# Optimization experiments

Measured on AMD Instinct MI355X. Metric: run time of the kernel, lower is better.

Reference implementation:

```python
import jax, jax.numpy as jnp
import numpy as np

# dims: T tokens, HID hidden, H heads, D head_dim, K conv kernel size
T, HID, H, D, K = 4096, 2048, 16, 128, 4
HD = H * D
EPS = 1e-6


def causal_conv(x, w):
    # depthwise causal conv: x [T, C], w [C, K]; y_t = sum_i w[:, i] * x_{t-K+1+i}
    xp = jnp.pad(x, ((K - 1, 0), (0, 0)))
    y = jnp.zeros_like(x)
    for i in range(K):  # small fixed kernel loop
        y = y + w[:, i] * xp[i:i + x.shape[0]]
    return y


def l2norm(x):
    return x * jax.lax.rsqrt(jnp.sum(x * x, -1, keepdims=True) + EPS)


def setup_inputs() -> dict:
    key = jax.random.key(0)
    ks = jax.random.split(key, 16)
    s = lambda n: 1.0 / np.sqrt(n)
    return {
        "hidden_states": jax.random.normal(ks[0], (T, HID), jnp.float32),
        "Wq": jax.random.normal(ks[1], (HID, HD), jnp.float32) * s(HID),
        "Wk": jax.random.normal(ks[2], (HID, HD), jnp.float32) * s(HID),
        "Wv": jax.random.normal(ks[3], (HID, HD), jnp.float32) * s(HID),
        "wq_conv": jax.random.normal(ks[4], (HD, K), jnp.float32) * s(K),
        "wk_conv": jax.random.normal(ks[5], (HD, K), jnp.float32) * s(K),
        "wv_conv": jax.random.normal(ks[6], (HD, K), jnp.float32) * s(K),
        "A_log": jax.random.uniform(ks[7], (H,), jnp.float32, 0.0, 0.5),
        "dt_bias": jax.random.normal(ks[8], (HD,), jnp.float32) * 0.1,
        "Wfa": jax.random.normal(ks[9], (HID, D), jnp.float32) * s(HID),
        "Wfb": jax.random.normal(ks[10], (D, HD), jnp.float32) * s(D),
        "Wb": jax.random.normal(ks[11], (HID, H), jnp.float32) * s(HID),
        "Wga": jax.random.normal(ks[12], (HID, D), jnp.float32) * s(HID),
        "Wgb": jax.random.normal(ks[13], (D, HD), jnp.float32) * s(D),
        "norm_w": jnp.ones((D,), jnp.float32),
        "Wo": jax.random.normal(ks[14], (HD, HID), jnp.float32) * s(HD),
    }


def reference(hidden_states, Wq, Wk, Wv, wq_conv, wk_conv, wv_conv, A_log,
              dt_bias, Wfa, Wfb, Wb, Wga, Wgb, norm_w, Wo):
    x = hidden_states
    # projections + short causal conv + SiLU
    q = jax.nn.silu(causal_conv(x @ Wq, wq_conv)).reshape(T, H, D)
    k = jax.nn.silu(causal_conv(x @ Wk, wk_conv)).reshape(T, H, D)
    v = jax.nn.silu(causal_conv(x @ Wv, wv_conv)).reshape(T, H, D)
    # fine-grained per-channel log-decay: g = -exp(A_log) * softplus(f + dt_bias), [T,H,D]
    f = (x @ Wfa) @ Wfb + dt_bias
    g = -(jnp.exp(A_log)[None, :, None]) * jax.nn.softplus(f.reshape(T, H, D))
    beta = jax.nn.sigmoid(x @ Wb)  # [T, H]
    q = l2norm(q)
    k = l2norm(k)
    scale = D ** -0.5

    def step(S, inp):  # S: [H, Dk, Dv]
        q_t, k_t, v_t, g_t, b_t = inp
        S = S * jnp.exp(g_t)[..., None]  # diagonal per-key-channel decay
        err = v_t - jnp.einsum('hkv,hk->hv', S, k_t)  # delta-rule error
        dv = b_t[:, None] * err  # beta gate
        S = S + k_t[:, :, None] * dv[:, None, :]
        o_t = jnp.einsum('hkv,hk->hv', S, q_t) * scale
        return S, o_t

    S0 = jnp.zeros((H, D, D), jnp.float32)
    _, o = jax.lax.scan(step, S0, (q, k, v, g, beta))  # o: [T, H, D]

    # gated RMSNorm then output projection
    gate = ((x @ Wga) @ Wgb).reshape(T, H, D)
    o = o * jax.lax.rsqrt(jnp.mean(o * o, -1, keepdims=True) + EPS)
    o = o * norm_w * jax.nn.silu(gate)
    return o.reshape(T, HD) @ Wo
```

## Files before the change

kernel.cpp:

```cpp
#include <hip/hip_runtime.h>
#include <hip/hip_bf16.h>
#include <math.h>

typedef __bf16 bf16_t;
typedef __bf16 bf16x8 __attribute__((ext_vector_type(8)));
typedef float  floatx4 __attribute__((ext_vector_type(4)));
typedef float  floatx2 __attribute__((ext_vector_type(2)));
typedef unsigned uintx4 __attribute__((ext_vector_type(4)));

constexpr int T_TOK = 4096;
constexpr int HID   = 2048;
constexpr int NH    = 16;
constexpr int DH    = 128;
constexpr int CH    = 2048;
constexpr int CHUNK = 16;
constexpr int NCH   = T_TOK / CHUNK;

__global__ __launch_bounds__(256) void cast_to_bf16(const float* __restrict__ in,
                                                    bf16_t* __restrict__ out, int n) {
  int i = (blockIdx.x * 256 + threadIdx.x) * 8;
  if (i >= n) return;
  float4 a = *(const float4*)(in + i);
  float4 b = *(const float4*)(in + i + 4);
  bf16x8 o;
  o[0]=(bf16_t)a.x; o[1]=(bf16_t)a.y; o[2]=(bf16_t)a.z; o[3]=(bf16_t)a.w;
  o[4]=(bf16_t)b.x; o[5]=(bf16_t)b.y; o[6]=(bf16_t)b.z; o[7]=(bf16_t)b.w;
  *(bf16x8*)(out + i) = o;
}

__global__ __launch_bounds__(256) void transpose_cast(const float* __restrict__ in,
                                                      bf16_t* __restrict__ out, int R, int C) {
  __shared__ float tile[32][33];
  int tx = threadIdx.x & 31;
  int ty = threadIdx.x >> 5;
  int r0 = blockIdx.x * 32;
  int c0 = blockIdx.y * 32;
#pragma unroll
  for (int i = 0; i < 4; i++) {
    int r = ty + i * 8;
    float v = 0.f;
    if (r0 + r < R && c0 + tx < C) v = in[(size_t)(r0 + r) * C + (c0 + tx)];
    tile[r][tx] = v;
  }
  __syncthreads();
#pragma unroll
  for (int i = 0; i < 4; i++) {
    int cr = ty + i * 8;
    if (c0 + cr < C && r0 + tx < R)
      out[(size_t)(c0 + cr) * R + (r0 + tx)] = (bf16_t)tile[tx][cr];
  }
}

template<bool OUT_BF16>
__global__ __launch_bounds__(256) void gemm_bf16(
    const bf16_t* __restrict__ A, int lda,
    const bf16_t* __restrict__ Bt, int ldb,
    void* __restrict__ Cv, int ldc, int M, int N, int K) {
  __shared__ bf16_t sA[128][40];
  __shared__ bf16_t sB[128][40];
  const int tid  = threadIdx.x;
  const int bm0  = blockIdx.x * 128;
  const int bn0  = blockIdx.y * 128;
  const int wave = tid >> 6;
  const int lane = tid & 63;
  const int wm   = (wave & 1) * 64;
  const int wn   = (wave >> 1) * 64;
  const int fm   = lane & 15;
  const int kq   = lane >> 4;

  floatx4 acc[4][4];
#pragma unroll
  for (int mi = 0; mi < 4; mi++)
#pragma unroll
    for (int ni = 0; ni < 4; ni++)
      acc[mi][ni] = (floatx4){0.f, 0.f, 0.f, 0.f};

  const int sr = tid >> 2;
  const int sk = (tid & 3) * 8;
  const bool bval0 = (bn0 + sr) < N;
  const bool bval1 = (bn0 + sr + 64) < N;
  const bf16_t* Ag0 = A + (size_t)(bm0 + sr) * lda + sk;
  const bf16_t* Ag1 = Ag0 + (size_t)64 * lda;
  const bf16_t* Bg0 = Bt + (size_t)(bn0 + sr) * ldb + sk;
  const bf16_t* Bg1 = Bg0 + (size_t)64 * ldb;

  for (int k0 = 0; k0 < K; k0 += 32) {
    float4 a0 = *(const float4*)(Ag0 + k0);
    float4 a1 = *(const float4*)(Ag1 + k0);
    float4 b0 = bval0 ? *(const float4*)(Bg0 + k0) : make_float4(0.f, 0.f, 0.f, 0.f);
    float4 b1 = bval1 ? *(const float4*)(Bg1 + k0) : make_float4(0.f, 0.f, 0.f, 0.f);
    __syncthreads();
    *(float4*)(&sA[sr][sk])      = a0;
    *(float4*)(&sA[sr + 64][sk]) = a1;
    *(float4*)(&sB[sr][sk])      = b0;
    *(float4*)(&sB[sr + 64][sk]) = b1;
    __syncthreads();
    bf16x8 afr[4], bfr[4];
#pragma unroll
    for (int i = 0; i < 4; i++) {
      afr[i] = *(const bf16x8*)(&sA[wm + i * 16 + fm][kq * 8]);
      bfr[i] = *(const bf16x8*)(&sB[wn + i * 16 + fm][kq * 8]);
    }
#pragma unroll
    for (int mi = 0; mi < 4; mi++)
#pragma unroll
      for (int ni = 0; ni < 4; ni++)
        acc[mi][ni] = __builtin_amdgcn_mfma_f32_16x16x32_bf16(afr[mi], bfr[ni], acc[mi][ni], 0, 0, 0);
  }

  const int rr = (lane >> 4) * 4;
#pragma unroll
  for (int mi = 0; mi < 4; mi++) {
#pragma unroll
    for (int r = 0; r < 4; r++) {
      const int row = bm0 + wm + mi * 16 + rr + r;
#pragma unroll
      for (int ni = 0; ni < 4; ni++) {
        const int col = bn0 + wn + ni * 16 + fm;
        if (col < N) {
          if constexpr (OUT_BF16)
            ((bf16_t*)Cv)[(size_t)row * ldc + col] = (bf16_t)acc[mi][ni][r];
          else
            ((float*)Cv)[(size_t)row * ldc + col] = acc[mi][ni][r];
        }
      }
    }
  }
}

template<bool L2NORM>
__global__ __launch_bounds__(256) void conv_silu(
    const bf16_t* __restrict__ raw, const float* __restrict__ wconv,
    bf16_t* __restrict__ out) {
  const int t   = blockIdx.x;
  const int tid = threadIdx.x;
  const int c0  = tid * 8;

  float w[8][4];
#pragma unroll
  for (int j = 0; j < 8; j++) {
    float4 t0 = *(const float4*)(wconv + (size_t)(c0 + j) * 4);
    w[j][0] = t0.x; w[j][1] = t0.y; w[j][2] = t0.z; w[j][3] = t0.w;
  }
  float a[8] = {};
#pragma unroll
  for (int i = 0; i < 4; i++) {
    int tr = t - 3 + i;
    if (tr < 0) continue;
    bf16x8 xr = *(const bf16x8*)(raw + (size_t)tr * CH + c0);
#pragma unroll
    for (int j = 0; j < 8; j++) a[j] += w[j][i] * (float)xr[j];
  }
  float s = 0.f;
#pragma unroll
  for (int j = 0; j < 8; j++) {
    a[j] = a[j] / (1.f + expf(-a[j]));
    s += a[j] * a[j];
  }
  float rs = 1.f;
  if constexpr (L2NORM) {
#pragma unroll
    for (int m = 1; m < 16; m <<= 1) s += __shfl_xor(s, m);
    rs = rsqrtf(s + 1e-6f);
  }
  bf16x8 r;
#pragma unroll
  for (int j = 0; j < 8; j++) r[j] = (bf16_t)(a[j] * rs);
  *(bf16x8*)(out + (size_t)t * CH + c0) = r;
}

__global__ __launch_bounds__(256) void gamma_beta(
    float* __restrict__ f_gam, const float* __restrict__ dt_bias,
    const float* __restrict__ A_log, float* __restrict__ beta_io) {
  const int t   = blockIdx.x;
  const int tid = threadIdx.x;
  const int c0  = tid * 8;
  const int h   = c0 >> 7;
  const float a_h = expf(A_log[h]);
  const size_t o0 = (size_t)t * CH + c0;
  float fv[8], db[8];
  { float4 f0 = *(const float4*)(f_gam + o0);   float4 f1 = *(const float4*)(f_gam + o0 + 4);
    fv[0]=f0.x; fv[1]=f0.y; fv[2]=f0.z; fv[3]=f0.w; fv[4]=f1.x; fv[5]=f1.y; fv[6]=f1.z; fv[7]=f1.w;
    float4 d0 = *(const float4*)(dt_bias + c0); float4 d1 = *(const float4*)(dt_bias + c0 + 4);
    db[0]=d0.x; db[1]=d0.y; db[2]=d0.z; db[3]=d0.w; db[4]=d1.x; db[5]=d1.y; db[6]=d1.z; db[7]=d1.w; }
  float og[8];
#pragma unroll
  for (int j = 0; j < 8; j++) {
    float f = fv[j] + db[j];
    float sp = (f > 20.f) ? f : log1pf(expf(f));
    og[j] = -a_h * sp;
  }
  *(float4*)(f_gam + o0)     = make_float4(og[0], og[1], og[2], og[3]);
  *(float4*)(f_gam + o0 + 4) = make_float4(og[4], og[5], og[6], og[7]);
  if (tid < NH) {
    float b = beta_io[(size_t)t * NH + tid];
    beta_io[(size_t)t * NH + tid] = 1.f / (1.f + expf(-b));
  }
}

template<int IMM>
__device__ __forceinline__ float swzf(float x) {
  return __builtin_bit_cast(float, __builtin_amdgcn_ds_swizzle(__builtin_bit_cast(int, x), IMM));
}
template<int CTRL>
__device__ __forceinline__ float dppadd(float x) {
  int v = __builtin_amdgcn_update_dpp(0, __builtin_bit_cast(int, x), CTRL, 0xF, 0xF, true);
  return x + __builtin_bit_cast(float, v);
}
__device__ __forceinline__ float cumsum16(float x) {
  x = dppadd<0x111>(x);
  x = dppadd<0x112>(x);
  x = dppadd<0x114>(x);
  x = dppadd<0x118>(x);
  return x;
}
__device__ __forceinline__ float bperm(int lane, float x) {
  return __builtin_bit_cast(float, __builtin_amdgcn_ds_bpermute(lane << 2, __builtin_bit_cast(int, x)));
}
__device__ __forceinline__ floatx2 bfpair(unsigned u) {
  floatx2 r;
  r[0] = __builtin_bit_cast(float, u << 16);
  r[1] = __builtin_bit_cast(float, u & 0xFFFF0000u);
  return r;
}

__global__ __launch_bounds__(64) void wy_prep(
    bf16_t* __restrict__ qn, bf16_t* __restrict__ kn,
    const float* __restrict__ gg, const float* __restrict__ beta,
    bf16_t* __restrict__ ktilT, float* __restrict__ Tm,
    bf16_t* __restrict__ MBf, float* __restrict__ ecT, float* __restrict__ e2T) {
  const int hc = blockIdx.x;
  const int h  = hc >> 8;
  const int c  = hc & 255;
  const int l  = threadIdx.x;
  const int tl = l & 15;
  const int gr = l >> 4;

  __shared__ bf16_t KldsT[128][24];
  __shared__ float  Wlds[16][17];
  __shared__ float  Mlds[16][17];
  __shared__ float  eclds[128], e2lds[128];
  __shared__ float  blds[16];

  const int kb0 = h * DH + gr * 8;
  const size_t rowoff = (size_t)(c * CHUNK + tl) * CH;

  if (gr == 0) blds[tl] = beta[(size_t)(c * CHUNK + tl) * NH + h];

  floatx4 wt = (floatx4){0.f, 0.f, 0.f, 0.f};
  floatx4 m  = (floatx4){0.f, 0.f, 0.f, 0.f};
  bf16x8 khs[4], qhs[4];
#pragma unroll
  for (int kb = 0; kb < 4; kb++) {
    const int ke = kb0 + kb * 32;
    float4 ga = *(const float4*)(gg + rowoff + ke);
    float4 gb = *(const float4*)(gg + rowoff + ke + 4);
    float cm[8] = {ga.x, ga.y, ga.z, ga.w, gb.x, gb.y, gb.z, gb.w};
    float lamh[8], lamt[8], ec[8], e2[8];
#pragma unroll
    for (int j = 0; j < 8; j++) {
      float cs   = cumsum16(cm[j]);
      float cmid = swzf<(7 << 5) | 0x10>(cs);
      lamh[j] = __expf(cs - cmid);
      lamt[j] = __expf(cmid - cs);
      ec[j]   = __expf(cmid);
      e2[j]   = swzf<(15 << 5) | 0x10>(lamh[j]);
    }
    if (tl == 0) {
#pragma unroll
      for (int j = 0; j < 8; j++) {
        eclds[kb * 32 + gr * 8 + j] = ec[j];
        e2lds[kb * 32 + gr * 8 + j] = e2[j];
      }
    }
    uint4 kr = *(const uint4*)(kn + rowoff + ke);
    uint4 qr = *(const uint4*)(qn + rowoff + ke);
    float kf[8], qf[8];
    { floatx2 a0 = bfpair(kr.x), a1 = bfpair(kr.y), a2 = bfpair(kr.z), a3 = bfpair(kr.w);
      kf[0]=a0[0];kf[1]=a0[1];kf[2]=a1[0];kf[3]=a1[1];kf[4]=a2[0];kf[5]=a2[1];kf[6]=a3[0];kf[7]=a3[1];
      floatx2 b0 = bfpair(qr.x), b1 = bfpair(qr.y), b2 = bfpair(qr.z), b3 = bfpair(qr.w);
      qf[0]=b0[0];qf[1]=b0[1];qf[2]=b1[0];qf[3]=b1[1];qf[4]=b2[0];qf[5]=b2[1];qf[6]=b3[0];qf[7]=b3[1]; }
    bf16x8 khat, ktil, qhat;
#pragma unroll
    for (int j = 0; j < 8; j++) {
      khat[j] = (bf16_t)(kf[j] * lamh[j]);
      ktil[j] = (bf16_t)(kf[j] * lamt[j]);
      qhat[j] = (bf16_t)(qf[j] * lamh[j]);
      khs[kb][j] = (bf16_t)(kf[j] * lamh[j] * ec[j]);
      qhs[kb][j] = (bf16_t)(qf[j] * lamh[j] * ec[j]);
    }
    wt = __builtin_amdgcn_mfma_f32_16x16x32_bf16(ktil, khat, wt, 0, 0, 0);
    m  = __builtin_amdgcn_mfma_f32_16x16x32_bf16(qhat, ktil, m,  0, 0, 0);
#pragma unroll
    for (int j = 0; j < 8; j++) KldsT[kb * 32 + gr * 8 + j][tl] = ktil[j];
  }
#pragma unroll
  for (int kb = 0; kb < 4; kb++) {
    *(uint4*)(kn + rowoff + kb0 + kb * 32) = __builtin_bit_cast(uint4, khs[kb]);
    *(uint4*)(qn + rowoff + kb0 + kb * 32) = __builtin_bit_cast(uint4, qhs[kb]);
  }
#pragma unroll
  for (int ri = 0; ri < 4; ri++) {
    Wlds[tl][4 * gr + ri] = wt[ri];
    Mlds[4 * gr + ri][tl] = (4 * gr + ri >= tl) ? m[ri] : 0.f;
  }
  {
    const int j = tl;
    float x[16];
#pragma unroll
    for (int t = 0; t < 16; t++) {
      float a = 0.f;
#pragma unroll
      for (int s = 0; s < 16; s++)
        if (s < t) a = fmaf(Wlds[t][s], x[s], a);
      x[t] = (t == j) ? 1.f : ((t > j) ? -blds[t] * a : 0.f);
    }
    if (gr == 0) {
      const float bj = blds[j];
#pragma unroll
      for (int t = 0; t < 16; t++)
        Tm[((size_t)hc * 16 + t) * 16 + j] = x[t] * bj;
    }
  }
  {
    uint4 mbo = {0, 0, 0, 0};
    if (gr < 2) {
      bf16x8 mm;
#pragma unroll
      for (int jj = 0; jj < 8; jj++) mm[jj] = (bf16_t)Mlds[tl][gr * 8 + jj];
      mbo = __builtin_bit_cast(uint4, mm);
    }
    ((uint4*)MBf)[(size_t)hc * 64 + l] = mbo;
  }
  for (int i = l; i < 128; i += 64) {
    uint4 a0 = *(const uint4*)&KldsT[i][0];
    uint4 a1 = *(const uint4*)&KldsT[i][8];
    bf16_t* dst = ktilT + ((size_t)hc * 128 + i) * 16;
    *(uint4*)dst = a0;
    *(uint4*)(dst + 8) = a1;
  }
  for (int i = l; i < 128; i += 64) {
    ecT[(size_t)hc * 128 + (i & 15) * 8 + (i >> 4)] = eclds[i];
    e2T[(size_t)hc * 128 + (i & 15) * 8 + (i >> 4)] = e2lds[i];
  }
}

__global__ __launch_bounds__(64, 1) void scan_wy2(
    const bf16_t* __restrict__ khsG, const bf16_t* __restrict__ qhsG,
    const bf16_t* __restrict__ vn, const bf16_t* __restrict__ ktilT,
    const float* __restrict__ Tm, const bf16_t* __restrict__ MBf,
    const float* __restrict__ ecT, const float* __restrict__ e2T,
    float* __restrict__ o) {
  const int h  = blockIdx.x >> 3;
  const int vt = blockIdx.x & 7;
  const int l  = threadIdx.x;
  const int tl = l & 15;
  const int gr = l >> 4;

  __shared__ float SldsT[16][132];
  __shared__ float DVlds[16][17];

  for (int i = l; i < 16 * 132; i += 64) (&SldsT[0][0])[i] = 0.f;

  float S[8][4];
#pragma unroll
  for (int kt = 0; kt < 8; kt++)
#pragma unroll
    for (int ri = 0; ri < 4; ri++) S[kt][ri] = 0.f;

  const int kb0 = h * DH + gr * 8;
  const int vb0 = h * DH + vt * 16 + gr * 4;
  const size_t hcBase = (size_t)h * NCH;
  constexpr float scale = 0.08838834764831845f;

  for (int c = 0; c < NCH; ++c) {
    const size_t rowoff = (size_t)(c * CHUNK + tl) * CH;
    const size_t hc = hcBase + c;

    uint4 khs[4], qhs[4];
#pragma unroll
    for (int kb = 0; kb < 4; kb++) {
      khs[kb] = *(const uint4*)(khsG + rowoff + kb0 + kb * 32);
      qhs[kb] = *(const uint4*)(qhsG + rowoff + kb0 + kb * 32);
    }
    uint2 vr = *(const uint2*)(vn + rowoff + vb0);
    const float* Trp = Tm + (hc * 16 + tl) * 16;
    floatx4 T0 = *(const floatx4*)(Trp);
    floatx4 T1 = *(const floatx4*)(Trp + 4);
    floatx4 T2 = *(const floatx4*)(Trp + 8);
    floatx4 T3 = *(const floatx4*)(Trp + 12);
    uint4 mb = ((const uint4*)MBf)[hc * 64 + l];
    uint4 ktb[8] = {};
    if (gr < 2) {
#pragma unroll
      for (int kt = 0; kt < 8; kt++)
        ktb[kt] = *(const uint4*)(ktilT + (hc * 128 + kt * 16 + tl) * 16 + gr * 8);
    }
    floatx4 ec0 = *(const floatx4*)(ecT + hc * 128 + tl * 8);
    floatx4 ec1 = *(const floatx4*)(ecT + hc * 128 + tl * 8 + 4);
    floatx4 e20 = *(const floatx4*)(e2T + hc * 128 + tl * 8);
    floatx4 e21 = *(const floatx4*)(e2T + hc * 128 + tl * 8 + 4);

    floatx4 p  = (floatx4){0.f, 0.f, 0.f, 0.f};
    floatx4 o1 = (floatx4){0.f, 0.f, 0.f, 0.f};
#pragma unroll
    for (int kb = 0; kb < 4; kb++) {
      float4 sa = *(const float4*)(&SldsT[tl][kb * 32 + gr * 8]);
      float4 sb = *(const float4*)(&SldsT[tl][kb * 32 + gr * 8 + 4]);
      bf16x8 s0a;
      s0a[0]=(bf16_t)sa.x; s0a[1]=(bf16_t)sa.y; s0a[2]=(bf16_t)sa.z; s0a[3]=(bf16_t)sa.w;
      s0a[4]=(bf16_t)sb.x; s0a[5]=(bf16_t)sb.y; s0a[6]=(bf16_t)sb.z; s0a[7]=(bf16_t)sb.w;
      p  = __builtin_amdgcn_mfma_f32_16x16x32_bf16(s0a, __builtin_bit_cast(bf16x8, khs[kb]), p,  0, 0, 0);
      o1 = __builtin_amdgcn_mfma_f32_16x16x32_bf16(s0a, __builtin_bit_cast(bf16x8, qhs[kb]), o1, 0, 0, 0);
    }
    float acc[4];
    { floatx2 v01 = bfpair(vr.x), v23 = bfpair(vr.y);
      acc[0] = v01[0] - p[0]; acc[1] = v01[1] - p[1];
      acc[2] = v23[0] - p[2]; acc[3] = v23[1] - p[3]; }
    float dv[4] = {0.f, 0.f, 0.f, 0.f};
#pragma unroll
    for (int s = 0; s < 16; s++) {
      const float ts = (s < 4) ? T0[s] : (s < 8) ? T1[s - 4] : (s < 12) ? T2[s - 8] : T3[s - 12];
#pragma unroll
      for (int ri = 0; ri < 4; ri++)
        dv[ri] = fmaf(ts, bperm((gr << 4) | s, acc[ri]), dv[ri]);
    }
#pragma unroll
    for (int ri = 0; ri < 4; ri++) DVlds[tl][4 * gr + ri] = dv[ri];
    bf16x8 dva = {};
    if (gr < 2) {
#pragma unroll
      for (int jj = 0; jj < 8; jj++) dva[jj] = (bf16_t)DVlds[gr * 8 + jj][tl];
    }
    floatx4 o2 = __builtin_amdgcn_mfma_f32_16x16x32_bf16(
        dva, __builtin_bit_cast(bf16x8, mb), (floatx4){0.f, 0.f, 0.f, 0.f}, 0, 0, 0);
    { float4 ov = make_float4((o1[0] + o2[0]) * scale, (o1[1] + o2[1]) * scale,
                              (o1[2] + o2[2]) * scale, (o1[3] + o2[3]) * scale);
      *(float4*)(o + rowoff + vb0) = ov; }
#pragma unroll
    for (int kt = 0; kt < 8; kt++) {
      const float ecK = (kt < 4) ? ec0[kt] : ec1[kt - 4];
      const float e2K = (kt < 4) ? e20[kt] : e21[kt - 4];
      floatx4 sa;
#pragma unroll
      for (int ri = 0; ri < 4; ri++) sa[ri] = ecK * S[kt][ri];
      sa = __builtin_amdgcn_mfma_f32_16x16x32_bf16(
          dva, __builtin_bit_cast(bf16x8, ktb[kt]), sa, 0, 0, 0);
#pragma unroll
      for (int ri = 0; ri < 4; ri++) S[kt][ri] = e2K * sa[ri];
    }
#pragma unroll
    for (int kt = 0; kt < 8; kt++)
#pragma unroll
      for (int ri = 0; ri < 4; ri++)
        SldsT[4 * gr + ri][kt * 16 + tl] = S[kt][ri];
  }
}

__global__ __launch_bounds__(256) void postprocess(
    const float* __restrict__ o, const bf16_t* __restrict__ gate,
    const float* __restrict__ norm_w, bf16_t* __restrict__ og) {
  const int t = blockIdx.x, tid = threadIdx.x;
  const int c0 = tid * 8, d0 = c0 & 127;
  const size_t o0 = (size_t)t * CH + c0;
  float ov[8], gv[8], nw[8];
  { float4 a = *(const float4*)(o + o0);    float4 b = *(const float4*)(o + o0 + 4);
    ov[0]=a.x; ov[1]=a.y; ov[2]=a.z; ov[3]=a.w; ov[4]=b.x; ov[5]=b.y; ov[6]=b.z; ov[7]=b.w;
    bf16x8 g8 = *(const bf16x8*)(gate + o0);
    for (int j = 0; j < 8; j++) gv[j] = (float)g8[j];
    float4 e = *(const float4*)(norm_w + d0); float4 f = *(const float4*)(norm_w + d0 + 4);
    nw[0]=e.x; nw[1]=e.y; nw[2]=e.z; nw[3]=e.w; nw[4]=f.x; nw[5]=f.y; nw[6]=f.z; nw[7]=f.w; }
  float ss = 0.f;
#pragma unroll
  for (int j = 0; j < 8; j++) ss += ov[j] * ov[j];
#pragma unroll
  for (int m = 1; m < 16; m <<= 1) ss += __shfl_xor(ss, m);
  const float rs = rsqrtf(ss * (1.f / 128.f) + 1e-6f);
  bf16x8 r;
#pragma unroll
  for (int j = 0; j < 8; j++) {
    float g = gv[j];
    float val = ov[j] * rs * nw[j] * (g / (1.f + expf(-g)));
    r[j] = (bf16_t)val;
  }
  *(bf16x8*)(og + o0) = r;
}

static inline void launch_gemm(const bf16_t* A, int lda, const bf16_t* Bt, int ldb,
                               void* C, int ldc, int M, int N, int K, bool obf16,
                               hipStream_t s) {
  dim3 grid(M / 128, (N + 127) / 128);
  if (obf16) gemm_bf16<true><<<grid, 256, 0, s>>>(A, lda, Bt, ldb, C, ldc, M, N, K);
  else       gemm_bf16<false><<<grid, 256, 0, s>>>(A, lda, Bt, ldb, C, ldc, M, N, K);
}

extern "C" void kernel_launch(void* const* d_in, const int* in_sizes, int n_in,
                              void* d_out, int out_size, void* d_ws, size_t ws_size,
                              hipStream_t stream) {
  const float* x       = (const float*)d_in[0];
  const float* Wq      = (const float*)d_in[1];
  const float* Wk      = (const float*)d_in[2];
  const float* Wv      = (const float*)d_in[3];
  const float* wqc     = (const float*)d_in[4];
  const float* wkc     = (const float*)d_in[5];
  const float* wvc     = (const float*)d_in[6];
  const float* A_log   = (const float*)d_in[7];
  const float* dt_bias = (const float*)d_in[8];
  const float* Wfa     = (const float*)d_in[9];
  const float* Wfb     = (const float*)d_in[10];
  const float* Wb      = (const float*)d_in[11];
  const float* Wga     = (const float*)d_in[12];
  const float* Wgb     = (const float*)d_in[13];
  const float* norm_w  = (const float*)d_in[14];
  const float* Wo      = (const float*)d_in[15];

  char* w = (char*)d_ws;
  size_t off = 0;
  auto give = [&](size_t bytes) -> void* {
    size_t cur = off;
    off = (off + bytes + 255) & ~(size_t)255;
    return (void*)(w + cur);
  };
  bf16_t* Wbig = (bf16_t*)give((size_t)CH * HID * 2);
  bf16_t* WfaT = (bf16_t*)give((size_t)128 * HID * 2);
  bf16_t* WgaT = (bf16_t*)give((size_t)128 * HID * 2);
  bf16_t* WfbT = (bf16_t*)give((size_t)CH * 128 * 2);
  bf16_t* WgbT = (bf16_t*)give((size_t)CH * 128 * 2);
  bf16_t* WbT  = (bf16_t*)give((size_t)NH * HID * 2);
  bf16_t* Ax   = (bf16_t*)give((size_t)T_TOK * HID * 2);
  bf16_t* raw0 = (bf16_t*)give((size_t)T_TOK * CH * 2);
  bf16_t* qnb  = (bf16_t*)give((size_t)T_TOK * CH * 2);
  bf16_t* knb  = (bf16_t*)give((size_t)T_TOK * CH * 2);
  bf16_t* vnb  = (bf16_t*)give((size_t)T_TOK * CH * 2);
  bf16_t* f1b  = (bf16_t*)give((size_t)T_TOK * 128 * 2);
  bf16_t* g1b  = (bf16_t*)give((size_t)T_TOK * 128 * 2);
  float*  fbuf = (float*)give((size_t)T_TOK * CH * 4);
  bf16_t* gateb= (bf16_t*)give((size_t)T_TOK * CH * 2);
  float*  betab= (float*)give((size_t)T_TOK * NH * 4);
  bf16_t* ktilT= (bf16_t*)give((size_t)NH * NCH * 128 * 16 * 2);
  float*  Tmat = (float*)give((size_t)NH * NCH * 256 * 4);
  bf16_t* MBf  = (bf16_t*)give((size_t)NH * NCH * 64 * 8 * 2);
  float*  ecTb = (float*)give((size_t)NH * NCH * 128 * 4);
  float*  e2Tb = (float*)give((size_t)NH * NCH * 128 * 4);
  float*  obuf = (float*)Ax;
  bf16_t* ogb  = qnb;

  auto tr = [&](const float* in, bf16_t* out, int R, int C) {
    transpose_cast<<<dim3((R + 31) / 32, (C + 31) / 32), 256, 0, stream>>>(in, out, R, C);
  };

  cast_to_bf16<<<dim3((T_TOK * HID) / 2048), 256, 0, stream>>>(x, Ax, T_TOK * HID);
  tr(Wfa, WfaT, HID, 128); tr(Wga, WgaT, HID, 128);
  tr(Wfb, WfbT, 128, CH);  tr(Wgb, WgbT, 128, CH);
  tr(Wb, WbT, HID, NH);

  tr(Wq, Wbig, HID, CH);
  launch_gemm(Ax, HID, Wbig, HID, raw0, CH, T_TOK, CH, HID, true, stream);
  conv_silu<true><<<dim3(T_TOK), 256, 0, stream>>>(raw0, wqc, qnb);
  tr(Wk, Wbig, HID, CH);
  launch_gemm(Ax, HID, Wbig, HID, raw0, CH, T_TOK, CH, HID, true, stream);
  conv_silu<true><<<dim3(T_TOK), 256, 0, stream>>>(raw0, wkc, knb);
  tr(Wv, Wbig, HID, CH);
  launch_gemm(Ax, HID, Wbig, HID, raw0, CH, T_TOK, CH, HID, true, stream);
  conv_silu<false><<<dim3(T_TOK), 256, 0, stream>>>(raw0, wvc, vnb);

  launch_gemm(Ax, HID, WfaT, HID, f1b, 128, T_TOK, 128, HID, true, stream);
  launch_gemm(Ax, HID, WgaT, HID, g1b, 128, T_TOK, 128, HID, true, stream);
  launch_gemm(Ax, HID, WbT, HID, betab, NH, T_TOK, NH, HID, false, stream);
  launch_gemm(f1b, 128, WfbT, 128, fbuf, CH, T_TOK, CH, 128, false, stream);
  launch_gemm(g1b, 128, WgbT, 128, gateb, CH, T_TOK, CH, 128, true, stream);
  gamma_beta<<<dim3(T_TOK), 256, 0, stream>>>(fbuf, dt_bias, A_log, betab);

  wy_prep<<<dim3(NH * NCH), 64, 0, stream>>>(qnb, knb, fbuf, betab,
                                             ktilT, Tmat, MBf, ecTb, e2Tb);
  scan_wy2<<<dim3(128), 64, 0, stream>>>(knb, qnb, vnb, ktilT, Tmat, MBf,
                                         ecTb, e2Tb, obuf);

  postprocess<<<dim3(T_TOK), 256, 0, stream>>>(obuf, gateb, norm_w, ogb);

  tr(Wo, Wbig, CH, HID);
  launch_gemm(ogb, CH, Wbig, CH, (float*)d_out, HID, T_TOK, HID, CH, false, stream);
}
```

Before: 1.125 ms.

## Warp-specialize scan with producer wave prefetching next chunk into double-buffered LDS

```diff
diff --git a/kernel.cpp b/kernel.cpp
--- a/kernel.cpp
+++ b/kernel.cpp
@@ -345,115 +345,150 @@
   }
 }
 
-__global__ __launch_bounds__(64, 1) void scan_wy2(
+__global__ __launch_bounds__(128, 1) void scan_wy3(
     const bf16_t* __restrict__ khsG, const bf16_t* __restrict__ qhsG,
     const bf16_t* __restrict__ vn, const bf16_t* __restrict__ ktilT,
     const float* __restrict__ Tm, const bf16_t* __restrict__ MBf,
     const float* __restrict__ ecT, const float* __restrict__ e2T,
     float* __restrict__ o) {
-  const int h  = blockIdx.x >> 3;
-  const int vt = blockIdx.x & 7;
-  const int l  = threadIdx.x;
-  const int tl = l & 15;
-  const int gr = l >> 4;
-
-  __shared__ float SldsT[16][132];
-  __shared__ float DVlds[16][17];
-
-  for (int i = l; i < 16 * 132; i += 64) (&SldsT[0][0])[i] = 0.f;
-
-  float S[8][4];
-#pragma unroll
-  for (int kt = 0; kt < 8; kt++)
-#pragma unroll
-    for (int ri = 0; ri < 4; ri++) S[kt][ri] = 0.f;
+  const int h   = blockIdx.x >> 3;
+  const int vt  = blockIdx.x & 7;
+  const int tid = threadIdx.x;
+  const int wid = tid >> 6;
+  const int l   = tid & 63;
+  const int tl  = l & 15;
+  const int gr  = l >> 4;
+
+  __shared__ uint4   sKQ[2][8][64];
+  __shared__ floatx4 sT[2][4][64];
+  __shared__ uint4   sMB[2][64];
+  __shared__ uint4   sKT[2][8][64];
+  __shared__ floatx4 sEC[2][4][64];
+  __shared__ uint2   sV[2][64];
+  __shared__ float   SldsT[16][132];
+  __shared__ float   DVlds[16][17];
 
   const int kb0 = h * DH + gr * 8;
   const int vb0 = h * DH + vt * 16 + gr * 4;
   const size_t hcBase = (size_t)h * NCH;
   constexpr float scale = 0.08838834764831845f;
 
-  for (int c = 0; c < NCH; ++c) {
+  auto produce = [&](int c, int b) {
     const size_t rowoff = (size_t)(c * CHUNK + tl) * CH;
     const size_t hc = hcBase + c;
-
-    uint4 khs[4], qhs[4];
+    uint4 kq[8];
 #pragma unroll
     for (int kb = 0; kb < 4; kb++) {
-      khs[kb] = *(const uint4*)(khsG + rowoff + kb0 + kb * 32);
-      qhs[kb] = *(const uint4*)(qhsG + rowoff + kb0 + kb * 32);
-    }
-    uint2 vr = *(const uint2*)(vn + rowoff + vb0);
+      kq[kb]     = *(const uint4*)(khsG + rowoff + kb0 + kb * 32);
+      kq[4 + kb] = *(const uint4*)(qhsG + rowoff + kb0 + kb * 32);
+    }
     const float* Trp = Tm + (hc * 16 + tl) * 16;
-    floatx4 T0 = *(const floatx4*)(Trp);
-    floatx4 T1 = *(const floatx4*)(Trp + 4);
-    floatx4 T2 = *(const floatx4*)(Trp + 8);
-    floatx4 T3 = *(const floatx4*)(Trp + 12);
-    uint4 mb = ((const uint4*)MBf)[hc * 64 + l];
-    uint4 ktb[8] = {};
-    if (gr < 2) {
+    floatx4 Tv[4];
+#pragma unroll
+    for (int j = 0; j < 4; j++) Tv[j] = *(const floatx4*)(Trp + 4 * j);
+    uint4 mbv = ((const uint4*)MBf)[hc * 64 + l];
+    const int g2 = gr & 1;
+    uint4 ktv[8];
+#pragma unroll
+    for (int kt = 0; kt < 8; kt++)
+      ktv[kt] = *(const uint4*)(ktilT + (hc * 128 + kt * 16 + tl) * 16 + g2 * 8);
+    floatx4 ecv[4];
+    ecv[0] = *(const floatx4*)(ecT + hc * 128 + tl * 8);
+    ecv[1] = *(const floatx4*)(ecT + hc * 128 + tl * 8 + 4);
+    ecv[2] = *(const floatx4*)(e2T + hc * 128 + tl * 8);
+    ecv[3] = *(const floatx4*)(e2T + hc * 128 + tl * 8 + 4);
+    uint2 vv = *(const uint2*)(vn + rowoff + vb0);
+#pragma unroll
+    for (int i = 0; i < 8; i++) sKQ[b][i][l] = kq[i];
+#pragma unroll
+    for (int j = 0; j < 4; j++) sT[b][j][l] = Tv[j];
+    sMB[b][l] = mbv;
+#pragma unroll
+    for (int i = 0; i < 8; i++) sKT[b][i][l] = ktv[i];
+#pragma unroll
+    for (int j = 0; j < 4; j++) sEC[b][j][l] = ecv[j];
+    sV[b][l] = vv;
+  };
+
+  float S[8][4];
+#pragma unroll
+  for (int kt = 0; kt < 8; kt++)
+#pragma unroll
+    for (int ri = 0; ri < 4; ri++) S[kt][ri] = 0.f;
+
+  if (wid == 1) {
+    produce(0, 0);
+  } else {
+    for (int i = l; i < 16 * 132; i += 64) (&SldsT[0][0])[i] = 0.f;
+  }
+  __syncthreads();
+
+  int cur = 0;
+  for (int c = 0; c < NCH; ++c) {
+    if (wid == 1) {
+      produce(c + 1 < NCH ? c + 1 : NCH - 1, cur ^ 1);
+    } else {
+      const size_t rowoff = (size_t)(c * CHUNK + tl) * CH;
+      floatx4 p  = (floatx4){0.f, 0.f, 0.f, 0.f};
+      floatx4 o1 = (floatx4){0.f, 0.f, 0.f, 0.f};
+#pragma unroll
+      for (int kb = 0; kb < 4; kb++) {
+        float4 sa = *(const float4*)(&SldsT[tl][kb * 32 + gr * 8]);
+        float4 sb = *(const float4*)(&SldsT[tl][kb * 32 + gr * 8 + 4]);
+        bf16x8 s0a;
+        s0a[0]=(bf16_t)sa.x; s0a[1]=(bf16_t)sa.y; s0a[2]=(bf16_t)sa.z; s0a[3]=(bf16_t)sa.w;
+        s0a[4]=(bf16_t)sb.x; s0a[5]=(bf16_t)sb.y; s0a[6]=(bf16_t)sb.z; s0a[7]=(bf16_t)sb.w;
+        p  = __builtin_amdgcn_mfma_f32_16x16x32_bf16(s0a, __builtin_bit_cast(bf16x8, sKQ[cur][kb][l]), p,  0, 0, 0);
+        o1 = __builtin_amdgcn_mfma_f32_16x16x32_bf16(s0a, __builtin_bit_cast(bf16x8, sKQ[cur][4 + kb][l]), o1, 0, 0, 0);
+      }
+      float acc[4];
+      { uint2 vr = sV[cur][l];
+        floatx2 v01 = bfpair(vr.x), v23 = bfpair(vr.y);
+        acc[0] = v01[0] - p[0]; acc[1] = v01[1] - p[1];
+        acc[2] = v23[0] - p[2]; acc[3] = v23[1] - p[3]; }
+      floatx4 T0 = sT[cur][0][l], T1 = sT[cur][1][l], T2 = sT[cur][2][l], T3 = sT[cur][3][l];
+      float dv[4] = {0.f, 0.f, 0.f, 0.f};
+#pragma unroll
+      for (int s = 0; s < 16; s++) {
+        const float ts = (s < 4) ? T0[s] : (s < 8) ? T1[s - 4] : (s < 12) ? T2[s - 8] : T3[s - 12];
+#pragma unroll
+        for (int ri = 0; ri < 4; ri++)
+          dv[ri] = fmaf(ts, bperm((gr << 4) | s, acc[ri]), dv[ri]);
+      }
+#pragma unroll
+      for (int ri = 0; ri < 4; ri++) DVlds[tl][4 * gr + ri] = dv[ri];
+      bf16x8 dva = {};
+      if (gr < 2) {
+#pragma unroll
+        for (int jj = 0; jj < 8; jj++) dva[jj] = (bf16_t)DVlds[gr * 8 + jj][tl];
+      }
+      floatx4 o2 = __builtin_amdgcn_mfma_f32_16x16x32_bf16(
+          dva, __builtin_bit_cast(bf16x8, sMB[cur][l]), (floatx4){0.f, 0.f, 0.f, 0.f}, 0, 0, 0);
+      { float4 ov = make_float4((o1[0] + o2[0]) * scale, (o1[1] + o2[1]) * scale,
+                                (o1[2] + o2[2]) * scale, (o1[3] + o2[3]) * scale);
+        *(float4*)(o + rowoff + vb0) = ov; }
+      floatx4 ec0 = sEC[cur][0][l], ec1 = sEC[cur][1][l];
+      floatx4 e20 = sEC[cur][2][l], e21 = sEC[cur][3][l];
+#pragma unroll
+      for (int kt = 0; kt < 8; kt++) {
+        const float ecK = (kt < 4) ? ec0[kt] : ec1[kt - 4];
+        const float e2K = (kt < 4) ? e20[kt] : e21[kt - 4];
+        floatx4 sa;
+#pragma unroll
+        for (int ri = 0; ri < 4; ri++) sa[ri] = ecK * S[kt][ri];
+        sa = __builtin_amdgcn_mfma_f32_16x16x32_bf16(
+            dva, __builtin_bit_cast(bf16x8, sKT[cur][kt][l]), sa, 0, 0, 0);
+#pragma unroll
+        for (int ri = 0; ri < 4; ri++) S[kt][ri] = e2K * sa[ri];
+      }
 #pragma unroll
       for (int kt = 0; kt < 8; kt++)
-        ktb[kt] = *(const uint4*)(ktilT + (hc * 128 + kt * 16 + tl) * 16 + gr * 8);
-    }
-    floatx4 ec0 = *(const floatx4*)(ecT + hc * 128 + tl * 8);
-    floatx4 ec1 = *(const floatx4*)(ecT + hc * 128 + tl * 8 + 4);
-    floatx4 e20 = *(const floatx4*)(e2T + hc * 128 + tl * 8);
-    floatx4 e21 = *(const floatx4*)(e2T + hc * 128 + tl * 8 + 4);
-
-    floatx4 p  = (floatx4){0.f, 0.f, 0.f, 0.f};
-    floatx4 o1 = (floatx4){0.f, 0.f, 0.f, 0.f};
-#pragma unroll
-    for (int kb = 0; kb < 4; kb++) {
-      float4 sa = *(const float4*)(&SldsT[tl][kb * 32 + gr * 8]);
-      float4 sb = *(const float4*)(&SldsT[tl][kb * 32 + gr * 8 + 4]);
-      bf16x8 s0a;
-      s0a[0]=(bf16_t)sa.x; s0a[1]=(bf16_t)sa.y; s0a[2]=(bf16_t)sa.z; s0a[3]=(bf16_t)sa.w;
-      s0a[4]=(bf16_t)sb.x; s0a[5]=(bf16_t)sb.y; s0a[6]=(bf16_t)sb.z; s0a[7]=(bf16_t)sb.w;
-      p  = __builtin_amdgcn_mfma_f32_16x16x32_bf16(s0a, __builtin_bit_cast(bf16x8, khs[kb]), p,  0, 0, 0);
-      o1 = __builtin_amdgcn_mfma_f32_16x16x32_bf16(s0a, __builtin_bit_cast(bf16x8, qhs[kb]), o1, 0, 0, 0);
-    }
-    float acc[4];
-    { floatx2 v01 = bfpair(vr.x), v23 = bfpair(vr.y);
-      acc[0] = v01[0] - p[0]; acc[1] = v01[1] - p[1];
-      acc[2] = v23[0] - p[2]; acc[3] = v23[1] - p[3]; }
-    float dv[4] = {0.f, 0.f, 0.f, 0.f};
-#pragma unroll
-    for (int s = 0; s < 16; s++) {
-      const float ts = (s < 4) ? T0[s] : (s < 8) ? T1[s - 4] : (s < 12) ? T2[s - 8] : T3[s - 12];
-#pragma unroll
-      for (int ri = 0; ri < 4; ri++)
-        dv[ri] = fmaf(ts, bperm((gr << 4) | s, acc[ri]), dv[ri]);
-    }
-#pragma unroll
-    for (int ri = 0; ri < 4; ri++) DVlds[tl][4 * gr + ri] = dv[ri];
-    bf16x8 dva = {};
-    if (gr < 2) {
-#pragma unroll
-      for (int jj = 0; jj < 8; jj++) dva[jj] = (bf16_t)DVlds[gr * 8 + jj][tl];
-    }
-    floatx4 o2 = __builtin_amdgcn_mfma_f32_16x16x32_bf16(
-        dva, __builtin_bit_cast(bf16x8, mb), (floatx4){0.f, 0.f, 0.f, 0.f}, 0, 0, 0);
-    { float4 ov = make_float4((o1[0] + o2[0]) * scale, (o1[1] + o2[1]) * scale,
-                              (o1[2] + o2[2]) * scale, (o1[3] + o2[3]) * scale);
-      *(float4*)(o + rowoff + vb0) = ov; }
-#pragma unroll
-    for (int kt = 0; kt < 8; kt++) {
-      const float ecK = (kt < 4) ? ec0[kt] : ec1[kt - 4];
-      const float e2K = (kt < 4) ? e20[kt] : e21[kt - 4];
-      floatx4 sa;
-#pragma unroll
-      for (int ri = 0; ri < 4; ri++) sa[ri] = ecK * S[kt][ri];
-      sa = __builtin_amdgcn_mfma_f32_16x16x32_bf16(
-          dva, __builtin_bit_cast(bf16x8, ktb[kt]), sa, 0, 0, 0);
-#pragma unroll
-      for (int ri = 0; ri < 4; ri++) S[kt][ri] = e2K * sa[ri];
-    }
-#pragma unroll
-    for (int kt = 0; kt < 8; kt++)
-#pragma unroll
-      for (int ri = 0; ri < 4; ri++)
-        SldsT[4 * gr + ri][kt * 16 + tl] = S[kt][ri];
+#pragma unroll
+        for (int ri = 0; ri < 4; ri++)
+          SldsT[4 * gr + ri][kt * 16 + tl] = S[kt][ri];
+    }
+    __syncthreads();
+    cur ^= 1;
   }
 }
 
@@ -573,8 +608,8 @@
 
   wy_prep<<<dim3(NH * NCH), 64, 0, stream>>>(qnb, knb, fbuf, betab,
                                              ktilT, Tmat, MBf, ecTb, e2Tb);
-  scan_wy2<<<dim3(128), 64, 0, stream>>>(knb, qnb, vnb, ktilT, Tmat, MBf,
-                                         ecTb, e2Tb, obuf);
+  scan_wy3<<<dim3(128), 128, 0, stream>>>(knb, qnb, vnb, ktilT, Tmat, MBf,
+                                          ecTb, e2Tb, obuf);
 
   postprocess<<<dim3(T_TOK), 256, 0, stream>>>(obuf, gateb, norm_w, ogb);
 
```

Result: faster. 1.070 ms (-4.9%).
